# Kernel tuning notes

Hardware: AMD Instinct MI355X
Metric: run time of the kernel (lower is better)

The kernel has to match this reference:

```python
import jax, jax.numpy as jnp
import numpy as np

N = 50000        # nodes
E = 800000       # directed edges (before self loops)
G = 1024         # graphs in batch
D = 128          # embedding_dim
H = 4            # attention heads
L = 3            # num_layers
NODE_DIM = 78
SLOPE = 0.2      # PyG GATConv leaky_relu negative slope
EPS = 1e-16


def setup_inputs() -> dict:
    key = jax.random.key(0)
    ks = jax.random.split(key, 20)
    s = lambda *sh: 1.0 / np.sqrt(sh[0])
    inp = {
        "x": jax.random.normal(ks[0], (N, NODE_DIM), jnp.float32),
        "edge_index": jax.random.randint(ks[1], (2, E), 0, N, jnp.int64),
        "batch": jnp.sort(jax.random.randint(ks[2], (N,), 0, G, jnp.int64)),
        # node_linear: Linear(78,128) -> ReLU -> Linear(128,128)
        "W1": jax.random.normal(ks[3], (NODE_DIM, D), jnp.float32) * s(NODE_DIM),
        "b1": jnp.zeros((D,), jnp.float32),
        "W2": jax.random.normal(ks[4], (D, D), jnp.float32) * s(D),
        "b2": jnp.zeros((D,), jnp.float32),
        # L stacked GATConv(D, D, heads=H, concat=False)
        "lin_w": jax.random.normal(ks[5], (L, D, H, D), jnp.float32) * s(D),
        "att_src": jax.random.normal(ks[6], (L, H, D), jnp.float32) * s(D),
        "att_dst": jax.random.normal(ks[7], (L, H, D), jnp.float32) * s(D),
        "conv_b": jnp.zeros((L, D), jnp.float32),
        # global_fc: Linear(128,1024) -> ReLU -> Dropout -> Linear(1024,128)
        "gW1": jax.random.normal(ks[8], (D, 1024), jnp.float32) * s(D),
        "gb1": jnp.zeros((1024,), jnp.float32),
        "gW2": jax.random.normal(ks[9], (1024, D), jnp.float32) * s(1024),
        "gb2": jnp.zeros((D,), jnp.float32),
    }
    return inp


def _gat_layer(x, src, dst, W, a_src, a_dst, b):
    # x: [N, D]; W: [D, H, D]
    h = jnp.einsum('nd,dhe->nhe', x, W)                    # [N, H, C]
    a_s = jnp.einsum('nhe,he->nh', h, a_src)               # [N, H]
    a_d = jnp.einsum('nhe,he->nh', h, a_dst)
    e = jax.nn.leaky_relu(a_s[src] + a_d[dst], SLOPE)      # [E', H]
    # segment softmax grouped by destination node
    m = jax.ops.segment_max(e, dst, num_segments=N)
    e = jnp.exp(e - m[dst])
    denom = jax.ops.segment_sum(e, dst, num_segments=N)
    alpha = e / (denom[dst] + EPS)                         # [E', H]
    out = jax.ops.segment_sum(h[src] * alpha[:, :, None], dst, num_segments=N)  # [N, H, C]
    return out.mean(axis=1) + b                            # concat=False: head mean


def reference(x, edge_index, batch, W1, b1, W2, b2, lin_w, att_src, att_dst,
              conv_b, gW1, gb1, gW2, gb2):
    # node_linear MLP
    h = jax.nn.relu(x @ W1 + b1) @ W2 + b2                 # [N, D]
    # add self loops (PyG GATConv default)
    loops = jnp.arange(N, dtype=edge_index.dtype)
    src = jnp.concatenate([edge_index[0], loops])
    dst = jnp.concatenate([edge_index[1], loops])
    for l in range(L):
        h = _gat_layer(h, src, dst, lin_w[l], att_src[l], att_dst[l], conv_b[l])
    # global mean pool per graph
    counts = jax.ops.segment_sum(jnp.ones((N,), h.dtype), batch, num_segments=G)
    pooled = jax.ops.segment_sum(h, batch, num_segments=G) / jnp.maximum(counts, 1.0)[:, None]
    # global_fc (dropout = identity at inference)
    return jax.nn.relu(pooled @ gW1 + gb1) @ gW2 + gb2     # [G, D]
```

## Files before the change

kernel.cpp:

```cpp
#include <hip/hip_runtime.h>
#include <hip/hip_bf16.h>

#define NN 50000
#define EE 800000
#define ET 850000
#define GG 1024
#define DD 128
#define HH 4
#define LL 3
#define ND 78
#define HD 512
#define K1P 96
#define SLOPE 0.2f
#define EPSV 1e-16f
#define SB 196
#define PADS 520

typedef __hip_bfloat16 bf16;
typedef __attribute__((ext_vector_type(8))) unsigned short u16x8;
typedef __attribute__((ext_vector_type(8))) short s16x8;
typedef __attribute__((ext_vector_type(4))) float f32x4;

__device__ __forceinline__ float b2f(bf16 v) { return __bfloat162float(v); }
__device__ __forceinline__ bf16 f2b(float v) { return __float2bfloat16(v); }
__device__ __forceinline__ float bu2f(unsigned short u) {
    return __uint_as_float(((unsigned)u) << 16);
}
__device__ __forceinline__ unsigned short f2bu(float f) {
    unsigned u = __float_as_uint(f);
    unsigned rounded = u + 0x7FFFu + ((u >> 16) & 1u);
    return (unsigned short)(rounded >> 16);
}
__device__ __forceinline__ float lrelu(float e) { return (e > 0.f) ? e : SLOPE * e; }

__global__ void detect_i(const unsigned* __restrict__ w, int* __restrict__ flag) {
    __shared__ int z;
    int t = threadIdx.x;
    if (t == 0) z = 0;
    __syncthreads();
    if (w[2 * t + 1] == 0u) atomicAdd(&z, 1);
    __syncthreads();
    if (t == 0) flag[0] = (z >= 200) ? 1 : 0;
}
__global__ void conv_i(const void* __restrict__ src, int* __restrict__ dst, int n,
                       const int* __restrict__ flag) {
    int i = blockIdx.x * 256 + threadIdx.x;
    if (i >= n) return;
    const int* s = (const int*)src;
    dst[i] = flag[0] ? s[2 * i] : s[i];
}

__global__ void xconv(const float* __restrict__ x, bf16* __restrict__ xb) {
    int idx = blockIdx.x * 256 + threadIdx.x;
    if (idx >= NN * K1P) return;
    int n = idx / K1P;
    int k = idx % K1P;
    xb[idx] = f2b((k < ND) ? x[(size_t)n * ND + k] : 0.f);
}
__global__ void nw_conv(const float* __restrict__ W1, const float* __restrict__ W2,
                        bf16* __restrict__ W1t, bf16* __restrict__ W2t) {
    int idx = blockIdx.x * 256 + threadIdx.x;
    if (idx < DD * K1P) {
        int c = idx / K1P, k = idx % K1P;
        W1t[idx] = f2b((k < ND) ? W1[(size_t)k * DD + c] : 0.f);
    }
    idx -= DD * K1P;
    if (idx >= 0 && idx < DD * DD) {
        int c = idx / DD, k = idx % DD;
        W2t[idx] = f2b(W2[(size_t)k * DD + c]);
    }
}

__global__ __launch_bounds__(256) void mlp_gemm1(const bf16* __restrict__ xb,
                                                 const bf16* __restrict__ W1t,
                                                 const float* __restrict__ b1,
                                                 bf16* __restrict__ ts) {
    int wid = (blockIdx.x * 256 + threadIdx.x) >> 6;
    if (wid >= NN / 16) return;
    int lane = threadIdx.x & 63;
    int r16 = lane & 15;
    int q = lane >> 4;
    const short* ab = (const short*)xb;
    const short* bb = (const short*)W1t;
    int arow = wid * 16 + r16;
    s16x8 afr[3];
#pragma unroll
    for (int c = 0; c < 3; c++) afr[c] = *(const s16x8*)(ab + (size_t)arow * K1P + c * 32 + q * 8);
#pragma unroll
    for (int nt = 0; nt < 8; nt++) {
        int brow = nt * 16 + r16;
        f32x4 acc = {0.f, 0.f, 0.f, 0.f};
#pragma unroll
        for (int c = 0; c < 3; c++) {
            s16x8 b = *(const s16x8*)(bb + (size_t)brow * K1P + c * 32 + q * 8);
            acc = __builtin_amdgcn_mfma_f32_16x16x32_bf16(afr[c], b, acc, 0, 0, 0);
        }
        int cc = nt * 16 + r16;
        float bias = b1[cc];
#pragma unroll
        for (int r = 0; r < 4; r++) {
            int row = wid * 16 + q * 4 + r;
            ts[(size_t)row * DD + cc] = f2b(fmaxf(acc[r] + bias, 0.f));
        }
    }
}

__global__ __launch_bounds__(256) void mlp_gemm2(const bf16* __restrict__ ts,
                                                 const bf16* __restrict__ W2t,
                                                 const float* __restrict__ b2,
                                                 bf16* __restrict__ h) {
    int wid = (blockIdx.x * 256 + threadIdx.x) >> 6;
    if (wid >= NN / 16) return;
    int lane = threadIdx.x & 63;
    int r16 = lane & 15;
    int q = lane >> 4;
    const short* ab = (const short*)ts;
    const short* bb = (const short*)W2t;
    int arow = wid * 16 + r16;
    s16x8 afr[4];
#pragma unroll
    for (int c = 0; c < 4; c++) afr[c] = *(const s16x8*)(ab + (size_t)arow * DD + c * 32 + q * 8);
#pragma unroll
    for (int nt = 0; nt < 8; nt++) {
        int brow = nt * 16 + r16;
        f32x4 acc = {0.f, 0.f, 0.f, 0.f};
#pragma unroll
        for (int c = 0; c < 4; c++) {
            s16x8 b = *(const s16x8*)(bb + (size_t)brow * DD + c * 32 + q * 8);
            acc = __builtin_amdgcn_mfma_f32_16x16x32_bf16(afr[c], b, acc, 0, 0, 0);
        }
        int cc = nt * 16 + r16;
        float bias = b2[cc];
#pragma unroll
        for (int r = 0; r < 4; r++) {
            int row = wid * 16 + q * 4 + r;
            h[(size_t)row * DD + cc] = f2b(acc[r] + bias);
        }
    }
}

__global__ void init_deg(int* deg) {
    int n = blockIdx.x * 256 + threadIdx.x;
    if (n < NN) deg[n] = 1;
}
__global__ void hist_edges(const int* __restrict__ ei, int* deg) {
    int e = blockIdx.x * 256 + threadIdx.x;
    if (e >= EE) return;
    int dst = ei[EE + e];
    if ((unsigned)dst < NN) atomicAdd(&deg[dst], 1);
}
__global__ __launch_bounds__(256) void block_sums(const int* __restrict__ deg, int* __restrict__ bsum) {
    __shared__ int part[256];
    int t = threadIdx.x;
    int i = blockIdx.x * 256 + t;
    part[t] = (i < NN) ? deg[i] : 0;
    __syncthreads();
    for (int off = 128; off > 0; off >>= 1) {
        if (t < off) part[t] += part[t + off];
        __syncthreads();
    }
    if (t == 0) bsum[blockIdx.x] = part[0];
}
__global__ __launch_bounds__(256) void scan_bsum(const int* __restrict__ bsum, int* __restrict__ boff,
                                                 int* __restrict__ start) {
    __shared__ int part[256];
    int t = threadIdx.x;
    part[t] = (t < SB) ? bsum[t] : 0;
    __syncthreads();
    for (int off = 1; off < 256; off <<= 1) {
        int add = (t >= off) ? part[t - off] : 0;
        __syncthreads();
        part[t] += add;
        __syncthreads();
    }
    if (t < SB) boff[t] = (t == 0) ? 0 : part[t - 1];
    if (t == 255) start[NN] = part[SB - 1];
}
__global__ __launch_bounds__(256) void scan_final(const int* __restrict__ deg, const int* __restrict__ boff,
                                                  int* __restrict__ start, int* __restrict__ cursor) {
    __shared__ int part[256];
    int t = threadIdx.x;
    int i = blockIdx.x * 256 + t;
    int v = (i < NN) ? deg[i] : 0;
    part[t] = v;
    __syncthreads();
    for (int off = 1; off < 256; off <<= 1) {
        int add = (t >= off) ? part[t - off] : 0;
        __syncthreads();
        part[t] += add;
        __syncthreads();
    }
    if (i < NN) {
        int ex = boff[blockIdx.x] + part[t] - v;
        start[i] = ex;
        cursor[i] = ex;
    }
}
__global__ void scatter_self(int* cursor, int* ssrc) {
    int n = blockIdx.x * 256 + threadIdx.x;
    if (n >= NN) return;
    int pos = atomicAdd(&cursor[n], 1);
    if ((unsigned)pos < ET) ssrc[pos] = n;
}
__global__ void scatter_edges(const int* __restrict__ ei, int* cursor, int* ssrc) {
    int e = blockIdx.x * 256 + threadIdx.x;
    if (e >= EE) return;
    int src = ei[e];
    int dst = ei[EE + e];
    if ((unsigned)dst >= NN) return;
    int pos = atomicAdd(&cursor[dst], 1);
    if ((unsigned)pos < ET) ssrc[pos] = ((unsigned)src < NN) ? src : 0;
}

__global__ void asd_w(const float* __restrict__ lin_w, const float* __restrict__ att_src,
                      const float* __restrict__ att_dst,
                      float* __restrict__ ws, float* __restrict__ wd) {
    int idx = blockIdx.x * 256 + threadIdx.x;
    if (idx >= LL * DD * HH) return;
    int l = idx / (DD * HH);
    int rem = idx % (DD * HH);
    int d = rem >> 2;
    int h = rem & 3;
    const float* wrow = lin_w + ((size_t)(l * DD + d) * HH + h) * DD;
    const float* as = att_src + (size_t)(l * HH + h) * DD;
    const float* ad = att_dst + (size_t)(l * HH + h) * DD;
    float s1 = 0.f, s2 = 0.f;
    for (int e = 0; e < DD; e++) { float w = wrow[e]; s1 += w * as[e]; s2 += w * ad[e]; }
    ws[idx] = s1;
    wd[idx] = s2;
}

__global__ void wt2_conv(const float* __restrict__ lin_w, bf16* __restrict__ Bt) {
    int idx = blockIdx.x * 256 + threadIdx.x;
    if (idx >= LL * DD * HD) return;
    int l = idx / (DD * HD);
    int rem = idx % (DD * HD);
    int c = rem / HD;
    int k = rem % HD;
    int h = k >> 7;
    int d = k & 127;
    Bt[idx] = f2b(lin_w[((size_t)(l * DD + d) * HH + h) * DD + c]);
}

__global__ void gw_conv(const float* __restrict__ gW1, const float* __restrict__ gW2,
                        bf16* __restrict__ gW1t, bf16* __restrict__ gW2t) {
    int idx = blockIdx.x * 256 + threadIdx.x;
    if (idx < 1024 * DD) {
        int c = idx / DD, k = idx % DD;
        gW1t[idx] = f2b(gW1[(size_t)k * 1024 + c]);
    }
    idx -= 1024 * DD;
    if (idx >= 0 && idx < DD * 1024) {
        int c = idx / 1024, k = idx % 1024;
        gW2t[idx] = f2b(gW2[(size_t)k * DD + c]);
    }
}

__global__ __launch_bounds__(256) void a_sd2(const bf16* __restrict__ h,
                                             const float* __restrict__ ws,
                                             const float* __restrict__ wd,
                                             float* __restrict__ a_s, float* __restrict__ a_d) {
    __shared__ float wsl[DD][HH];
    __shared__ float wdl[DD][HH];
    int t = threadIdx.x;
    for (int i = t; i < DD * HH; i += 256) { wsl[i >> 2][i & 3] = ws[i]; wdl[i >> 2][i & 3] = wd[i]; }
    __syncthreads();
    int n = blockIdx.x * 256 + t;
    if (n >= NN) return;
    const u16x8* row = (const u16x8*)((const unsigned short*)h + (size_t)n * DD);
    float s1[HH] = {0.f, 0.f, 0.f, 0.f};
    float s2[HH] = {0.f, 0.f, 0.f, 0.f};
    for (int c = 0; c < 16; c++) {
        u16x8 v = row[c];
#pragma unroll
        for (int k = 0; k < 8; k++) {
            int d = c * 8 + k;
            float f = bu2f(v[k]);
#pragma unroll
            for (int hh = 0; hh < HH; hh++) {
                s1[hh] += f * wsl[d][hh];
                s2[hh] += f * wdl[d][hh];
            }
        }
    }
#pragma unroll
    for (int hh = 0; hh < HH; hh++) {
        a_s[n * HH + hh] = s1[hh];
        a_d[n * HH + hh] = s2[hh];
    }
}

__global__ __launch_bounds__(1024) void agg_gemm(const int* __restrict__ start,
                                                 const int* __restrict__ ssrc,
                                                 const float* __restrict__ a_s,
                                                 const float* __restrict__ a_d,
                                                 const bf16* __restrict__ h,
                                                 const bf16* __restrict__ Bt,
                                                 const float* __restrict__ conv_b,
                                                 bf16* __restrict__ hnext) {
    __shared__ short aggL[16 * PADS];
    __shared__ float wlds[16][64][HH];
    __shared__ float mxl[16][HH];
    __shared__ float invl[16][HH];
    int wv = threadIdx.x >> 6;
    int lane = threadIdx.x & 63;
    int node16 = blockIdx.x * 16;
    int node = node16 + wv;

    int s0 = start[node];
    int deg = start[node + 1] - s0;
    int sidx = (lane < deg) ? ssrc[s0 + lane] : 0;

    {
        int jj = lane & 15;
        int hh = lane >> 4;
        float ad = a_d[node * HH + hh];
        float ec[4];
        float mx = -1e30f;
#pragma unroll
        for (int k = 0; k < 4; k++) {
            int j = jj + k * 16;
            float e = -1e30f;
            if (j < deg) {
                int s = __shfl(sidx, j);
                e = lrelu(a_s[s * HH + hh] + ad);
            }
            ec[k] = e;
            mx = fmaxf(mx, e);
        }
        for (int j = jj + 64; j < deg; j += 16) {
            int s = ssrc[s0 + j];
            mx = fmaxf(mx, lrelu(a_s[s * HH + hh] + ad));
        }
#pragma unroll
        for (int off = 1; off < 16; off <<= 1) mx = fmaxf(mx, __shfl_xor(mx, off));
        float den = 0.f;
#pragma unroll
        for (int k = 0; k < 4; k++) {
            int j = jj + k * 16;
            if (j < deg) {
                float ww = __expf(ec[k] - mx);
                den += ww;
                wlds[wv][j][hh] = ww;
            }
        }
        for (int j = jj + 64; j < deg; j += 16) {
            int s = ssrc[s0 + j];
            den += __expf(lrelu(a_s[s * HH + hh] + ad) - mx);
        }
#pragma unroll
        for (int off = 1; off < 16; off <<= 1) den += __shfl_xor(den, off);
        if (jj == 0) {
            invl[wv][hh] = 1.f / (den + EPSV);
            mxl[wv][hh] = mx;
        }
    }
    __syncthreads();

    const unsigned* hu = (const unsigned*)h;
    float acc[HH][2];
#pragma unroll
    for (int hh = 0; hh < HH; hh++) { acc[hh][0] = 0.f; acc[hh][1] = 0.f; }

    auto fmaEdge = [&](float4 w4, unsigned hv) {
        float v0 = bu2f((unsigned short)(hv & 0xFFFFu));
        float v1 = bu2f((unsigned short)(hv >> 16));
        acc[0][0] += w4.x * v0; acc[0][1] += w4.x * v1;
        acc[1][0] += w4.y * v0; acc[1][1] += w4.y * v1;
        acc[2][0] += w4.z * v0; acc[2][1] += w4.z * v1;
        acc[3][0] += w4.w * v0; acc[3][1] += w4.w * v1;
    };

    {
        int m = (deg > 64) ? 64 : deg;
        int j = 0;
        for (; j + 4 <= m; j += 4) {
            int sA = __shfl(sidx, j);
            int sB = __shfl(sidx, j + 1);
            int sC = __shfl(sidx, j + 2);
            int sD = __shfl(sidx, j + 3);
            float4 wA = *(const float4*)wlds[wv][j];
            float4 wB = *(const float4*)wlds[wv][j + 1];
            float4 wC = *(const float4*)wlds[wv][j + 2];
            float4 wD = *(const float4*)wlds[wv][j + 3];
            unsigned hA = hu[(size_t)sA * (DD / 2) + lane];
            unsigned hB = hu[(size_t)sB * (DD / 2) + lane];
            unsigned hC = hu[(size_t)sC * (DD / 2) + lane];
            unsigned hD = hu[(size_t)sD * (DD / 2) + lane];
            fmaEdge(wA, hA);
            fmaEdge(wB, hB);
            fmaEdge(wC, hC);
            fmaEdge(wD, hD);
        }
        for (; j < m; j++) {
            int s = __shfl(sidx, j);
            float4 w4 = *(const float4*)wlds[wv][j];
            unsigned hv = hu[(size_t)s * (DD / 2) + lane];
            fmaEdge(w4, hv);
        }
        for (j = 64; j < deg; j++) {
            int s = ssrc[s0 + j];
            float4 as4 = *(const float4*)(a_s + (size_t)s * HH);
            float4 ad4 = *(const float4*)(a_d + (size_t)node * HH);
            float4 w4;
            w4.x = __expf(lrelu(as4.x + ad4.x) - mxl[wv][0]);
            w4.y = __expf(lrelu(as4.y + ad4.y) - mxl[wv][1]);
            w4.z = __expf(lrelu(as4.z + ad4.z) - mxl[wv][2]);
            w4.w = __expf(lrelu(as4.w + ad4.w) - mxl[wv][3]);
            unsigned hv = hu[(size_t)s * (DD / 2) + lane];
            fmaEdge(w4, hv);
        }
    }
    float4 inv4 = *(const float4*)invl[wv];
    float invs[HH] = {inv4.x, inv4.y, inv4.z, inv4.w};
    unsigned* aggU = (unsigned*)aggL;
#pragma unroll
    for (int hh = 0; hh < HH; hh++) {
        unsigned packed = (unsigned)f2bu(acc[hh][0] * invs[hh]) |
                          ((unsigned)f2bu(acc[hh][1] * invs[hh]) << 16);
        aggU[wv * (PADS / 2) + hh * (DD / 2) + lane] = packed;
    }
    __syncthreads();

    if (wv < 8) {
        int nt = wv;
        int r16 = lane & 15;
        int q = lane >> 4;
        const short* bb = (const short*)Bt;
        int brow = nt * 16 + r16;
        f32x4 gacc = {0.f, 0.f, 0.f, 0.f};
#pragma unroll
        for (int c = 0; c < 16; c++) {
            s16x8 a = *(const s16x8*)(aggL + r16 * PADS + c * 32 + q * 8);
            s16x8 b = *(const s16x8*)(bb + (size_t)brow * HD + c * 32 + q * 8);
            gacc = __builtin_amdgcn_mfma_f32_16x16x32_bf16(a, b, gacc, 0, 0, 0);
        }
        int cc = nt * 16 + r16;
        float bias = conv_b[cc];
#pragma unroll
        for (int r = 0; r < 4; r++) {
            int row = node16 + q * 4 + r;
            hnext[(size_t)row * DD + cc] = f2b(0.25f * gacc[r] + bias);
        }
    }
}

__global__ void pool_init(float* pooled, int* counts) {
    int idx = blockIdx.x * 256 + threadIdx.x;
    if (idx < GG * DD) pooled[idx] = 0.f;
    if (idx < GG) counts[idx] = 0;
}
__global__ void pool_count(const int* __restrict__ batch, int* counts) {
    int n = blockIdx.x * 256 + threadIdx.x;
    if (n >= NN) return;
    int g = batch[n];
    if ((unsigned)g < GG) atomicAdd(&counts[g], 1);
}
__global__ __launch_bounds__(256) void pool_accum2(const bf16* __restrict__ h,
                                                   const int* __restrict__ batch,
                                                   float* pooled) {
    int t = threadIdx.x;
    int d = t & 127;
    int half = t >> 7;
    int n0 = blockIdx.x * 64 + half * 32;
    int n1 = n0 + 32; if (n1 > NN) n1 = NN;
    float acc = 0.f;
    int cur = -1;
    for (int n = n0; n < n1; n++) {
        int g = batch[n];
        if ((unsigned)g >= GG) continue;
        if (g != cur) {
            if (cur >= 0) atomicAdd(&pooled[cur * DD + d], acc);
            acc = 0.f; cur = g;
        }
        acc += b2f(h[(size_t)n * DD + d]);
    }
    if (cur >= 0) atomicAdd(&pooled[cur * DD + d], acc);
}
__global__ void pooled2bf(const float* __restrict__ pooled, const int* __restrict__ counts,
                          bf16* __restrict__ pbf) {
    int idx = blockIdx.x * 256 + threadIdx.x;
    if (idx >= GG * DD) return;
    int g = idx >> 7;
    int c = counts[g]; if (c < 1) c = 1;
    pbf[idx] = f2b(pooled[idx] / (float)c);
}

__global__ __launch_bounds__(256) void fc1_mfma(const bf16* __restrict__ pbf,
                                                const bf16* __restrict__ gW1t,
                                                const float* __restrict__ gb1,
                                                bf16* __restrict__ t1) {
    int wid = (blockIdx.x * 256 + threadIdx.x) >> 6;
    int lane = threadIdx.x & 63;
    int mt = wid >> 6;
    int nt = wid & 63;
    int r16 = lane & 15;
    int q = lane >> 4;
    const short* ab = (const short*)pbf;
    const short* bb = (const short*)gW1t;
    f32x4 acc = {0.f, 0.f, 0.f, 0.f};
    int arow = mt * 16 + r16;
    int brow = nt * 16 + r16;
#pragma unroll
    for (int c = 0; c < 4; c++) {
        s16x8 a = *(const s16x8*)(ab + (size_t)arow * DD + c * 32 + q * 8);
        s16x8 b = *(const s16x8*)(bb + (size_t)brow * DD + c * 32 + q * 8);
        acc = __builtin_amdgcn_mfma_f32_16x16x32_bf16(a, b, acc, 0, 0, 0);
    }
    int cc = nt * 16 + r16;
    float bias = gb1[cc];
#pragma unroll
    for (int r = 0; r < 4; r++) {
        int row = mt * 16 + q * 4 + r;
        t1[(size_t)row * 1024 + cc] = f2b(fmaxf(acc[r] + bias, 0.f));
    }
}

__global__ __launch_bounds__(256) void fc2_mfma(const bf16* __restrict__ t1,
                                                const bf16* __restrict__ gW2t,
                                                const float* __restrict__ gb2,
                                                float* __restrict__ out) {
    int wid = (blockIdx.x * 256 + threadIdx.x) >> 6;
    int lane = threadIdx.x & 63;
    int mt = wid >> 3;
    int nt = wid & 7;
    int r16 = lane & 15;
    int q = lane >> 4;
    const short* ab = (const short*)t1;
    const short* bb = (const short*)gW2t;
    f32x4 acc = {0.f, 0.f, 0.f, 0.f};
    int arow = mt * 16 + r16;
    int brow = nt * 16 + r16;
#pragma unroll
    for (int c = 0; c < 32; c++) {
        s16x8 a = *(const s16x8*)(ab + (size_t)arow * 1024 + c * 32 + q * 8);
        s16x8 b = *(const s16x8*)(bb + (size_t)brow * 1024 + c * 32 + q * 8);
        acc = __builtin_amdgcn_mfma_f32_16x16x32_bf16(a, b, acc, 0, 0, 0);
    }
    int cc = nt * 16 + r16;
    float bias = gb2[cc];
#pragma unroll
    for (int r = 0; r < 4; r++) {
        int row = mt * 16 + q * 4 + r;
        out[(size_t)row * DD + cc] = acc[r] + bias;
    }
}

__global__ void sentinel_only(float* out, int hostcode) {
    if (threadIdx.x == 0 && blockIdx.x == 0) out[0] = (float)hostcode;
}

extern "C" void kernel_launch(void* const* d_in, const int* in_sizes, int n_in,
                              void* d_out, int out_size, void* d_ws, size_t ws_size,
                              hipStream_t stream) {
    float* out = (float*)d_out;

    static const int expect[15] = {3900000, 1600000, 50000, 9984, 128, 16384, 128,
                                   196608, 1536, 1536, 384, 131072, 1024, 131072, 128};
    int hostcode = 0;
    if (n_in != 15) hostcode = 21099;
    else for (int i = 0; i < 15; i++) if (in_sizes[i] != expect[i]) { hostcode = 21000 + i; break; }
    if (hostcode == 0 && out_size != GG * DD) hostcode = 35000;

    const float* x       = (const float*)d_in[0];
    const float* W1      = (const float*)d_in[3];
    const float* b1      = (const float*)d_in[4];
    const float* W2      = (const float*)d_in[5];
    const float* b2      = (const float*)d_in[6];
    const float* lin_w   = (const float*)d_in[7];
    const float* att_src = (const float*)d_in[8];
    const float* att_dst = (const float*)d_in[9];
    const float* conv_b  = (const float*)d_in[10];
    const float* gW1     = (const float*)d_in[11];
    const float* gb1     = (const float*)d_in[12];
    const float* gW2     = (const float*)d_in[13];
    const float* gb2     = (const float*)d_in[14];

    char* p = (char*)d_ws;
    auto alloc = [&](size_t bytes) { void* q = (void*)p; p += (bytes + 255) & ~(size_t)255; return q; };
    int*   flags  = (int*)alloc(4 * 4);
    int*   ei32   = (int*)alloc((size_t)2 * EE * 4);
    int*   bat32  = (int*)alloc((size_t)NN * 4);
    bf16*  xb     = (bf16*)alloc((size_t)NN * K1P * 2);
    bf16*  W1tb   = (bf16*)alloc((size_t)DD * K1P * 2);
    bf16*  W2tb   = (bf16*)alloc((size_t)DD * DD * 2);
    bf16*  tsbuf  = (bf16*)alloc((size_t)NN * DD * 2);
    bf16*  hA     = (bf16*)alloc((size_t)NN * DD * 2);
    bf16*  hB     = (bf16*)alloc((size_t)NN * DD * 2);
    bf16*  Bt     = (bf16*)alloc((size_t)LL * DD * HD * 2);
    float* wsbuf  = (float*)alloc((size_t)LL * DD * HH * 4);
    float* wdbuf  = (float*)alloc((size_t)LL * DD * HH * 4);
    float* a_s    = (float*)alloc((size_t)NN * HH * 4);
    float* a_d    = (float*)alloc((size_t)NN * HH * 4);
    int*   deg    = (int*)alloc((size_t)NN * 4);
    int*   start  = (int*)alloc((size_t)(NN + 1) * 4);
    int*   cursor = (int*)alloc((size_t)NN * 4);
    int*   ssrc   = (int*)alloc((size_t)ET * 4);
    int*   bsum   = (int*)alloc((size_t)SB * 4);
    int*   boff   = (int*)alloc((size_t)SB * 4);
    float* pooled = (float*)alloc((size_t)GG * DD * 4);
    int*   counts = (int*)alloc((size_t)GG * 4);
    bf16*  pbf    = (bf16*)alloc((size_t)GG * DD * 2);
    bf16*  gW1t   = (bf16*)alloc((size_t)1024 * DD * 2);
    bf16*  gW2t   = (bf16*)alloc((size_t)DD * 1024 * 2);
    bf16*  t1buf  = (bf16*)alloc((size_t)GG * 1024 * 2);
    size_t need = (size_t)(p - (char*)d_ws);
    if (hostcode == 0 && ws_size < need) hostcode = 34000;

    if (hostcode != 0) {
        sentinel_only<<<1, 64, 0, stream>>>(out, hostcode);
        return;
    }

    detect_i<<<1, 256, 0, stream>>>((const unsigned*)d_in[1], flags + 0);
    detect_i<<<1, 256, 0, stream>>>((const unsigned*)d_in[2], flags + 1);
    conv_i<<<(2 * EE + 255) / 256, 256, 0, stream>>>(d_in[1], ei32, 2 * EE, flags + 0);
    conv_i<<<(NN + 255) / 256, 256, 0, stream>>>(d_in[2], bat32, NN, flags + 1);

    xconv<<<((size_t)NN * K1P + 255) / 256, 256, 0, stream>>>(x, xb);
    nw_conv<<<(DD * K1P + DD * DD + 255) / 256, 256, 0, stream>>>(W1, W2, W1tb, W2tb);
    mlp_gemm1<<<(NN / 16 * 64 + 255) / 256, 256, 0, stream>>>(xb, W1tb, b1, tsbuf);
    mlp_gemm2<<<(NN / 16 * 64 + 255) / 256, 256, 0, stream>>>(tsbuf, W2tb, b2, hA);

    asd_w<<<(LL * DD * HH + 255) / 256, 256, 0, stream>>>(lin_w, att_src, att_dst, wsbuf, wdbuf);
    wt2_conv<<<(LL * DD * HD + 255) / 256, 256, 0, stream>>>(lin_w, Bt);
    gw_conv<<<(2 * 1024 * DD + 255) / 256, 256, 0, stream>>>(gW1, gW2, gW1t, gW2t);
    init_deg<<<(NN + 255) / 256, 256, 0, stream>>>(deg);
    hist_edges<<<(EE + 255) / 256, 256, 0, stream>>>(ei32, deg);
    block_sums<<<SB, 256, 0, stream>>>(deg, bsum);
    scan_bsum<<<1, 256, 0, stream>>>(bsum, boff, start);
    scan_final<<<SB, 256, 0, stream>>>(deg, boff, start, cursor);
    scatter_self<<<(NN + 255) / 256, 256, 0, stream>>>(cursor, ssrc);
    scatter_edges<<<(EE + 255) / 256, 256, 0, stream>>>(ei32, cursor, ssrc);

    bf16* hin = hA;
    bf16* hout = hB;
    for (int l = 0; l < LL; l++) {
        a_sd2<<<(NN + 255) / 256, 256, 0, stream>>>(hin, wsbuf + l * DD * HH, wdbuf + l * DD * HH, a_s, a_d);
        agg_gemm<<<NN / 16, 1024, 0, stream>>>(start, ssrc, a_s, a_d, hin,
                                               Bt + (size_t)l * DD * HD, conv_b + l * DD, hout);
        bf16* tmp = hin; hin = hout; hout = tmp;
    }
    pool_init<<<(GG * DD + 255) / 256, 256, 0, stream>>>(pooled, counts);
    pool_count<<<(NN + 255) / 256, 256, 0, stream>>>(bat32, counts);
    pool_accum2<<<(NN + 63) / 64, 256, 0, stream>>>(hin, bat32, pooled);
    pooled2bf<<<(GG * DD + 255) / 256, 256, 0, stream>>>(pooled, counts, pbf);
    fc1_mfma<<<(64 * 64) / 4, 256, 0, stream>>>(pbf, gW1t, gb1, t1buf);
    fc2_mfma<<<(64 * 8) / 4, 256, 0, stream>>>(t1buf, gW2t, gb2, out);
}
```

Measured before the change: 598.8 us.

## Fuse prep and scatter launches and batch neighbor gathers in GAT aggregation

Several small preprocessing kernels (weight conversions, attention-weight precompute, pooled/degree init) are merged into one prep_misc launch. Degree init is folded into edge conversion, and self-loop plus edge scatter are merged into one kernel, all to cut launch overhead. In agg_gemm the per-edge gather now issues 8 independent loads via readlane byte offsets and accumulates in packed f32x2 FMAs. It also drops a block barrier and the deg guard on weight writes, and adds a launch_bounds occupancy hint. The unguarded weight writes and chunk padding rely on out-of-range entries giving zero weights, and the removed barrier assumes each wave only reads its own LDS slice.

```diff
diff --git a/kernel.cpp b/kernel.cpp
--- a/kernel.cpp
+++ b/kernel.cpp
@@ -20,6 +20,7 @@
 typedef __attribute__((ext_vector_type(8))) unsigned short u16x8;
 typedef __attribute__((ext_vector_type(8))) short s16x8;
 typedef __attribute__((ext_vector_type(4))) float f32x4;
+typedef __attribute__((ext_vector_type(2))) float f32x2;
 
 __device__ __forceinline__ float b2f(bf16 v) { return __bfloat162float(v); }
 __device__ __forceinline__ bf16 f2b(float v) { return __float2bfloat16(v); }
@@ -49,25 +50,90 @@
     const int* s = (const int*)src;
     dst[i] = flag[0] ? s[2 * i] : s[i];
 }
-
-__global__ void xconv(const float* __restrict__ x, bf16* __restrict__ xb) {
+__global__ void conv_edges(const void* __restrict__ src, int* __restrict__ dst,
+                           const int* __restrict__ flag, int* __restrict__ deg) {
+    int i = blockIdx.x * 256 + threadIdx.x;
+    if (i < NN) deg[i] = 1;
+    if (i >= 2 * EE) return;
+    const int* s = (const int*)src;
+    dst[i] = flag[0] ? s[2 * i] : s[i];
+}
+
+#define PRE0 (NN * K1P)
+#define PRE1 (PRE0 + DD * K1P + DD * DD)
+#define PRE2 (PRE1 + LL * DD * HD)
+#define PRE3 (PRE2 + 2 * 1024 * DD)
+#define PRE4 (PRE3 + LL * DD * HH)
+#define PRE5 (PRE4 + GG * DD + GG)
+__global__ void prep_misc(const float* __restrict__ x, const float* __restrict__ W1,
+                          const float* __restrict__ W2, const float* __restrict__ lin_w,
+                          const float* __restrict__ att_src, const float* __restrict__ att_dst,
+                          const float* __restrict__ gW1, const float* __restrict__ gW2,
+                          bf16* __restrict__ xb, bf16* __restrict__ W1t, bf16* __restrict__ W2t,
+                          bf16* __restrict__ Bt, float* __restrict__ ws, float* __restrict__ wd,
+                          bf16* __restrict__ gW1t, bf16* __restrict__ gW2t,
+                          float* __restrict__ pooled, int* __restrict__ counts) {
     int idx = blockIdx.x * 256 + threadIdx.x;
-    if (idx >= NN * K1P) return;
-    int n = idx / K1P;
-    int k = idx % K1P;
-    xb[idx] = f2b((k < ND) ? x[(size_t)n * ND + k] : 0.f);
-}
-__global__ void nw_conv(const float* __restrict__ W1, const float* __restrict__ W2,
-                        bf16* __restrict__ W1t, bf16* __restrict__ W2t) {
-    int idx = blockIdx.x * 256 + threadIdx.x;
-    if (idx < DD * K1P) {
-        int c = idx / K1P, k = idx % K1P;
-        W1t[idx] = f2b((k < ND) ? W1[(size_t)k * DD + c] : 0.f);
-    }
-    idx -= DD * K1P;
-    if (idx >= 0 && idx < DD * DD) {
-        int c = idx / DD, k = idx % DD;
-        W2t[idx] = f2b(W2[(size_t)k * DD + c]);
+    if (idx < PRE0) {
+        int n = idx / K1P;
+        int k = idx % K1P;
+        xb[idx] = f2b((k < ND) ? x[(size_t)n * ND + k] : 0.f);
+        return;
+    }
+    if (idx < PRE1) {
+        idx -= PRE0;
+        if (idx < DD * K1P) {
+            int c = idx / K1P, k = idx % K1P;
+            W1t[idx] = f2b((k < ND) ? W1[(size_t)k * DD + c] : 0.f);
+        } else {
+            idx -= DD * K1P;
+            int c = idx / DD, k = idx % DD;
+            W2t[idx] = f2b(W2[(size_t)k * DD + c]);
+        }
+        return;
+    }
+    if (idx < PRE2) {
+        idx -= PRE1;
+        int l = idx / (DD * HD);
+        int rem = idx % (DD * HD);
+        int c = rem / HD;
+        int k = rem % HD;
+        int h = k >> 7;
+        int d = k & 127;
+        Bt[idx] = f2b(lin_w[((size_t)(l * DD + d) * HH + h) * DD + c]);
+        return;
+    }
+    if (idx < PRE3) {
+        idx -= PRE2;
+        if (idx < 1024 * DD) {
+            int c = idx / DD, k = idx % DD;
+            gW1t[idx] = f2b(gW1[(size_t)k * 1024 + c]);
+        } else {
+            idx -= 1024 * DD;
+            int c = idx / 1024, k = idx % 1024;
+            gW2t[idx] = f2b(gW2[(size_t)k * DD + c]);
+        }
+        return;
+    }
+    if (idx < PRE4) {
+        idx -= PRE3;
+        int l = idx / (DD * HH);
+        int rem = idx % (DD * HH);
+        int d = rem >> 2;
+        int h = rem & 3;
+        const float* wrow = lin_w + ((size_t)(l * DD + d) * HH + h) * DD;
+        const float* as = att_src + (size_t)(l * HH + h) * DD;
+        const float* ad = att_dst + (size_t)(l * HH + h) * DD;
+        float s1 = 0.f, s2 = 0.f;
+        for (int e = 0; e < DD; e++) { float w = wrow[e]; s1 += w * as[e]; s2 += w * ad[e]; }
+        ws[idx] = s1;
+        wd[idx] = s2;
+        return;
+    }
+    if (idx < PRE5) {
+        idx -= PRE4;
+        if (idx < GG * DD) pooled[idx] = 0.f;
+        if (idx < GG) counts[idx] = 0;
     }
 }
 
@@ -139,10 +205,6 @@
     }
 }
 
-__global__ void init_deg(int* deg) {
-    int n = blockIdx.x * 256 + threadIdx.x;
-    if (n < NN) deg[n] = 1;
-}
 __global__ void hist_edges(const int* __restrict__ ei, int* deg) {
     int e = blockIdx.x * 256 + threadIdx.x;
     if (e >= EE) return;
@@ -196,64 +258,20 @@
         cursor[i] = ex;
     }
 }
-__global__ void scatter_self(int* cursor, int* ssrc) {
-    int n = blockIdx.x * 256 + threadIdx.x;
-    if (n >= NN) return;
-    int pos = atomicAdd(&cursor[n], 1);
-    if ((unsigned)pos < ET) ssrc[pos] = n;
-}
-__global__ void scatter_edges(const int* __restrict__ ei, int* cursor, int* ssrc) {
-    int e = blockIdx.x * 256 + threadIdx.x;
+__global__ void scatter_all(const int* __restrict__ ei, int* cursor, int* ssrc) {
+    int i = blockIdx.x * 256 + threadIdx.x;
+    if (i < NN) {
+        int pos = atomicAdd(&cursor[i], 1);
+        if ((unsigned)pos < ET) ssrc[pos] = i;
+        return;
+    }
+    int e = i - NN;
     if (e >= EE) return;
     int src = ei[e];
     int dst = ei[EE + e];
     if ((unsigned)dst >= NN) return;
     int pos = atomicAdd(&cursor[dst], 1);
     if ((unsigned)pos < ET) ssrc[pos] = ((unsigned)src < NN) ? src : 0;
-}
-
-__global__ void asd_w(const float* __restrict__ lin_w, const float* __restrict__ att_src,
-                      const float* __restrict__ att_dst,
-                      float* __restrict__ ws, float* __restrict__ wd) {
-    int idx = blockIdx.x * 256 + threadIdx.x;
-    if (idx >= LL * DD * HH) return;
-    int l = idx / (DD * HH);
-    int rem = idx % (DD * HH);
-    int d = rem >> 2;
-    int h = rem & 3;
-    const float* wrow = lin_w + ((size_t)(l * DD + d) * HH + h) * DD;
-    const float* as = att_src + (size_t)(l * HH + h) * DD;
-    const float* ad = att_dst + (size_t)(l * HH + h) * DD;
-    float s1 = 0.f, s2 = 0.f;
-    for (int e = 0; e < DD; e++) { float w = wrow[e]; s1 += w * as[e]; s2 += w * ad[e]; }
-    ws[idx] = s1;
-    wd[idx] = s2;
-}
-
-__global__ void wt2_conv(const float* __restrict__ lin_w, bf16* __restrict__ Bt) {
-    int idx = blockIdx.x * 256 + threadIdx.x;
-    if (idx >= LL * DD * HD) return;
-    int l = idx / (DD * HD);
-    int rem = idx % (DD * HD);
-    int c = rem / HD;
-    int k = rem % HD;
-    int h = k >> 7;
-    int d = k & 127;
-    Bt[idx] = f2b(lin_w[((size_t)(l * DD + d) * HH + h) * DD + c]);
-}
-
-__global__ void gw_conv(const float* __restrict__ gW1, const float* __restrict__ gW2,
-                        bf16* __restrict__ gW1t, bf16* __restrict__ gW2t) {
-    int idx = blockIdx.x * 256 + threadIdx.x;
-    if (idx < 1024 * DD) {
-        int c = idx / DD, k = idx % DD;
-        gW1t[idx] = f2b(gW1[(size_t)k * 1024 + c]);
-    }
-    idx -= 1024 * DD;
-    if (idx >= 0 && idx < DD * 1024) {
-        int c = idx / 1024, k = idx % 1024;
-        gW2t[idx] = f2b(gW2[(size_t)k * DD + c]);
-    }
 }
 
 __global__ __launch_bounds__(256) void a_sd2(const bf16* __restrict__ h,
@@ -290,14 +308,14 @@
     }
 }
 
-__global__ __launch_bounds__(1024) void agg_gemm(const int* __restrict__ start,
-                                                 const int* __restrict__ ssrc,
-                                                 const float* __restrict__ a_s,
-                                                 const float* __restrict__ a_d,
-                                                 const bf16* __restrict__ h,
-                                                 const bf16* __restrict__ Bt,
-                                                 const float* __restrict__ conv_b,
-                                                 bf16* __restrict__ hnext) {
+__global__ __launch_bounds__(1024, 8) void agg_gemm(const int* __restrict__ start,
+                                                    const int* __restrict__ ssrc,
+                                                    const float* __restrict__ a_s,
+                                                    const float* __restrict__ a_d,
+                                                    const bf16* __restrict__ h,
+                                                    const bf16* __restrict__ Bt,
+                                                    const float* __restrict__ conv_b,
+                                                    bf16* __restrict__ hnext) {
     __shared__ short aggL[16 * PADS];
     __shared__ float wlds[16][64][HH];
     __shared__ float mxl[16][HH];
@@ -310,6 +328,7 @@
     int s0 = start[node];
     int deg = start[node + 1] - s0;
     int sidx = (lane < deg) ? ssrc[s0 + lane] : 0;
+    int soff = sidx << 8;
 
     {
         int jj = lane & 15;
@@ -338,11 +357,9 @@
 #pragma unroll
         for (int k = 0; k < 4; k++) {
             int j = jj + k * 16;
-            if (j < deg) {
-                float ww = __expf(ec[k] - mx);
-                den += ww;
-                wlds[wv][j][hh] = ww;
-            }
+            float ww = __expf(ec[k] - mx);
+            den += ww;
+            wlds[wv][j][hh] = ww;
         }
         for (int j = jj + 64; j < deg; j += 16) {
             int s = ssrc[s0 + j];
@@ -355,69 +372,61 @@
             mxl[wv][hh] = mx;
         }
     }
-    __syncthreads();
-
-    const unsigned* hu = (const unsigned*)h;
-    float acc[HH][2];
-#pragma unroll
-    for (int hh = 0; hh < HH; hh++) { acc[hh][0] = 0.f; acc[hh][1] = 0.f; }
-
-    auto fmaEdge = [&](float4 w4, unsigned hv) {
-        float v0 = bu2f((unsigned short)(hv & 0xFFFFu));
-        float v1 = bu2f((unsigned short)(hv >> 16));
-        acc[0][0] += w4.x * v0; acc[0][1] += w4.x * v1;
-        acc[1][0] += w4.y * v0; acc[1][1] += w4.y * v1;
-        acc[2][0] += w4.z * v0; acc[2][1] += w4.z * v1;
-        acc[3][0] += w4.w * v0; acc[3][1] += w4.w * v1;
-    };
-
-    {
-        int m = (deg > 64) ? 64 : deg;
-        int j = 0;
-        for (; j + 4 <= m; j += 4) {
-            int sA = __shfl(sidx, j);
-            int sB = __shfl(sidx, j + 1);
-            int sC = __shfl(sidx, j + 2);
-            int sD = __shfl(sidx, j + 3);
-            float4 wA = *(const float4*)wlds[wv][j];
-            float4 wB = *(const float4*)wlds[wv][j + 1];
-            float4 wC = *(const float4*)wlds[wv][j + 2];
-            float4 wD = *(const float4*)wlds[wv][j + 3];
-            unsigned hA = hu[(size_t)sA * (DD / 2) + lane];
-            unsigned hB = hu[(size_t)sB * (DD / 2) + lane];
-            unsigned hC = hu[(size_t)sC * (DD / 2) + lane];
-            unsigned hD = hu[(size_t)sD * (DD / 2) + lane];
-            fmaEdge(wA, hA);
-            fmaEdge(wB, hB);
-            fmaEdge(wC, hC);
-            fmaEdge(wD, hD);
-        }
-        for (; j < m; j++) {
-            int s = __shfl(sidx, j);
-            float4 w4 = *(const float4*)wlds[wv][j];
-            unsigned hv = hu[(size_t)s * (DD / 2) + lane];
-            fmaEdge(w4, hv);
-        }
-        for (j = 64; j < deg; j++) {
-            int s = ssrc[s0 + j];
-            float4 as4 = *(const float4*)(a_s + (size_t)s * HH);
-            float4 ad4 = *(const float4*)(a_d + (size_t)node * HH);
-            float4 w4;
-            w4.x = __expf(lrelu(as4.x + ad4.x) - mxl[wv][0]);
-            w4.y = __expf(lrelu(as4.y + ad4.y) - mxl[wv][1]);
-            w4.z = __expf(lrelu(as4.z + ad4.z) - mxl[wv][2]);
-            w4.w = __expf(lrelu(as4.w + ad4.w) - mxl[wv][3]);
-            unsigned hv = hu[(size_t)s * (DD / 2) + lane];
-            fmaEdge(w4, hv);
-        }
-    }
+
+    const char* hb = (const char*)h;
+    int lb4 = lane << 2;
+    f32x2 acc2[HH];
+#pragma unroll
+    for (int hh = 0; hh < HH; hh++) acc2[hh] = (f32x2){0.f, 0.f};
+
+    int m = (deg > 64) ? 64 : deg;
+    int nch = (m + 7) >> 3;
+    for (int c = 0; c < nch; c++) {
+        int j = c * 8;
+        unsigned hv[8];
+#pragma unroll
+        for (int k = 0; k < 8; k++) {
+            int bo = __builtin_amdgcn_readlane(soff, j + k) + lb4;
+            hv[k] = *(const unsigned*)(hb + bo);
+        }
+#pragma unroll
+        for (int k = 0; k < 8; k++) {
+            float4 w4 = *(const float4*)wlds[wv][j + k];
+            f32x2 v;
+            v.x = __uint_as_float(hv[k] << 16);
+            v.y = __uint_as_float(hv[k] & 0xffff0000u);
+            acc2[0] += v * w4.x;
+            acc2[1] += v * w4.y;
+            acc2[2] += v * w4.z;
+            acc2[3] += v * w4.w;
+        }
+    }
+    for (int j = 64; j < deg; j++) {
+        int s = ssrc[s0 + j];
+        float4 as4 = *(const float4*)(a_s + (size_t)s * HH);
+        float4 ad4 = *(const float4*)(a_d + (size_t)node * HH);
+        float4 w4;
+        w4.x = __expf(lrelu(as4.x + ad4.x) - mxl[wv][0]);
+        w4.y = __expf(lrelu(as4.y + ad4.y) - mxl[wv][1]);
+        w4.z = __expf(lrelu(as4.z + ad4.z) - mxl[wv][2]);
+        w4.w = __expf(lrelu(as4.w + ad4.w) - mxl[wv][3]);
+        unsigned hv = *(const unsigned*)(hb + ((size_t)s << 8) + lb4);
+        f32x2 v;
+        v.x = __uint_as_float(hv << 16);
+        v.y = __uint_as_float(hv & 0xffff0000u);
+        acc2[0] += v * w4.x;
+        acc2[1] += v * w4.y;
+        acc2[2] += v * w4.z;
+        acc2[3] += v * w4.w;
+    }
+
     float4 inv4 = *(const float4*)invl[wv];
     float invs[HH] = {inv4.x, inv4.y, inv4.z, inv4.w};
     unsigned* aggU = (unsigned*)aggL;
 #pragma unroll
     for (int hh = 0; hh < HH; hh++) {
-        unsigned packed = (unsigned)f2bu(acc[hh][0] * invs[hh]) |
-                          ((unsigned)f2bu(acc[hh][1] * invs[hh]) << 16);
+        unsigned packed = (unsigned)f2bu(acc2[hh].x * invs[hh]) |
+                          ((unsigned)f2bu(acc2[hh].y * invs[hh]) << 16);
         aggU[wv * (PADS / 2) + hh * (DD / 2) + lane] = packed;
     }
     __syncthreads();
@@ -445,11 +454,6 @@
     }
 }
 
-__global__ void pool_init(float* pooled, int* counts) {
-    int idx = blockIdx.x * 256 + threadIdx.x;
-    if (idx < GG * DD) pooled[idx] = 0.f;
-    if (idx < GG) counts[idx] = 0;
-}
 __global__ void pool_count(const int* __restrict__ batch, int* counts) {
     int n = blockIdx.x * 256 + threadIdx.x;
     if (n >= NN) return;
@@ -614,24 +618,21 @@
 
     detect_i<<<1, 256, 0, stream>>>((const unsigned*)d_in[1], flags + 0);
     detect_i<<<1, 256, 0, stream>>>((const unsigned*)d_in[2], flags + 1);
-    conv_i<<<(2 * EE + 255) / 256, 256, 0, stream>>>(d_in[1], ei32, 2 * EE, flags + 0);
+    conv_edges<<<(2 * EE + 255) / 256, 256, 0, stream>>>(d_in[1], ei32, flags + 0, deg);
     conv_i<<<(NN + 255) / 256, 256, 0, stream>>>(d_in[2], bat32, NN, flags + 1);
 
-    xconv<<<((size_t)NN * K1P + 255) / 256, 256, 0, stream>>>(x, xb);
-    nw_conv<<<(DD * K1P + DD * DD + 255) / 256, 256, 0, stream>>>(W1, W2, W1tb, W2tb);
+    prep_misc<<<PRE5 / 256, 256, 0, stream>>>(x, W1, W2, lin_w, att_src, att_dst, gW1, gW2,
+                                              xb, W1tb, W2tb, Bt, wsbuf, wdbuf, gW1t, gW2t,
+                                              pooled, counts);
+
     mlp_gemm1<<<(NN / 16 * 64 + 255) / 256, 256, 0, stream>>>(xb, W1tb, b1, tsbuf);
     mlp_gemm2<<<(NN / 16 * 64 + 255) / 256, 256, 0, stream>>>(tsbuf, W2tb, b2, hA);
 
-    asd_w<<<(LL * DD * HH + 255) / 256, 256, 0, stream>>>(lin_w, att_src, att_dst, wsbuf, wdbuf);
-    wt2_conv<<<(LL * DD * HD + 255) / 256, 256, 0, stream>>>(lin_w, Bt);
-    gw_conv<<<(2 * 1024 * DD + 255) / 256, 256, 0, stream>>>(gW1, gW2, gW1t, gW2t);
-    init_deg<<<(NN + 255) / 256, 256, 0, stream>>>(deg);
     hist_edges<<<(EE + 255) / 256, 256, 0, stream>>>(ei32, deg);
     block_sums<<<SB, 256, 0, stream>>>(deg, bsum);
     scan_bsum<<<1, 256, 0, stream>>>(bsum, boff, start);
     scan_final<<<SB, 256, 0, stream>>>(deg, boff, start, cursor);
-    scatter_self<<<(NN + 255) / 256, 256, 0, stream>>>(cursor, ssrc);
-    scatter_edges<<<(EE + 255) / 256, 256, 0, stream>>>(ei32, cursor, ssrc);
+    scatter_all<<<(NN + EE + 255) / 256, 256, 0, stream>>>(ei32, cursor, ssrc);
 
     bf16* hin = hA;
     bf16* hout = hB;
@@ -641,7 +642,6 @@
                                                Bt + (size_t)l * DD * HD, conv_b + l * DD, hout);
         bf16* tmp = hin; hin = hout; hout = tmp;
     }
-    pool_init<<<(GG * DD + 255) / 256, 256, 0, stream>>>(pooled, counts);
     pool_count<<<(NN + 255) / 256, 256, 0, stream>>>(bat32, counts);
     pool_accum2<<<(NN + 63) / 64, 256, 0, stream>>>(hin, bat32, pooled);
     pooled2bf<<<(GG * DD + 255) / 256, 256, 0, stream>>>(pooled, counts, pbf);
```

Result: faster. 576.4 us (-3.7%).
